# Optimization experiments

Hardware: AMD Instinct MI355X
Metric: run time of the kernel (lower is better)

Reference implementation:

```python
import jax, jax.numpy as jnp
import numpy as np

B, N_KERNELS, IN_DIM, UNITS = 512, 128, 1024, 1024

def setup_inputs() -> dict:
    key = jax.random.key(0)
    k1, k2 = jax.random.split(key)
    x = jax.random.normal(k1, (B, N_KERNELS, IN_DIM), dtype=jnp.float32)
    kernels = jax.random.normal(k2, (N_KERNELS, IN_DIM, UNITS), dtype=jnp.float32) * 0.02
    return {"x": x, "kernels": kernels}

def reference(x, kernels):
    # Original loops over n_kernels doing x[:, i:i+1, :] @ kernels[i] then softplus.
    # Note: the original's K.bias_add return value is discarded, so bias never
    # affects the output; the faithful math has no bias term.
    # Batched GEMM over the position axis k: [B,K,I] x [K,I,O] -> [B,K,O]
    out = jax.nn.softplus(jnp.einsum('bki,kio->bko', x, kernels))
    return out
```

## Files before the change

### kernel.cpp

```cpp
#include <hip/hip_runtime.h>

#define NKER  128
#define INDIM 1024
#define UNITS 1024

typedef __attribute__((ext_vector_type(8)))  short          bf16x8;
typedef __attribute__((ext_vector_type(4)))  float          f32x4;
typedef __attribute__((ext_vector_type(4)))  unsigned short u16x4;
typedef __attribute__((ext_vector_type(8)))  unsigned short u16x8;

#define LGKM0   asm volatile("s_waitcnt lgkmcnt(0)" ::: "memory")
#define BAR()   __builtin_amdgcn_s_barrier()
#define SCHED0  __builtin_amdgcn_sched_barrier(0)

__device__ __forceinline__ unsigned short f2bf(float f) {
    return __builtin_bit_cast(unsigned short, static_cast<__bf16>(f));
}

__device__ __forceinline__ int swzidx(int r, int k) {
    return r * 32 + ((((k >> 3) ^ ((r >> 1) & 3)) << 3) | (k & 7));
}

__global__ void __launch_bounds__(512, 2)
dense_local(const float* __restrict__ X, const float* __restrict__ Kn,
            float* __restrict__ Out)
{
    __shared__ __align__(16) unsigned short lA[2][2][256 * 32];
    __shared__ __align__(16) unsigned short lB[2][2][128 * 32];

    const int bid  = blockIdx.x;
    const int wg   = (bid & 7) * 256 + (bid >> 3);
    const int kidx = wg >> 4;
    const int tile = wg & 15;
    const int mt   = tile >> 3;
    const int nt   = tile & 7;

    const int t   = threadIdx.x;
    const int l   = t & 63;
    const int w   = t >> 6;
    const int wm  = w >> 1;
    const int wn  = w & 1;
    const int l15 = l & 15, g = l >> 4;

    const size_t MROW = (size_t)NKER * INDIM;

    const float* Abase = X   + (size_t)mt * 256 * MROW + (size_t)kidx * INDIM;
    const float* Bbase = Kn  + (size_t)kidx * INDIM * UNITS + nt * 128;
    float*       Cbase = Out + (size_t)mt * 256 * MROW + (size_t)kidx * UNITS + nt * 128;

    const int ar0 = t >> 3;
    const int ak4 = (t & 7) << 2;
    const int bn  = t & 127;
    const int bkh = t >> 7;

    const float* aP = Abase + (size_t)ar0 * MROW + ak4;
    const float* bP = Bbase + (size_t)bkh * 8 * UNITS + bn;

    f32x4 acc[4][4];
#pragma unroll
    for (int mi = 0; mi < 4; ++mi)
#pragma unroll
        for (int ni = 0; ni < 4; ++ni)
            acc[mi][ni] = f32x4{0.f, 0.f, 0.f, 0.f};

    f32x4 SA[4][2];
    float SB[2][8];

    auto issueA = [&]() {
#pragma unroll
        for (int p = 0; p < 4; ++p)
#pragma unroll
            for (int s = 0; s < 2; ++s)
                SA[p][s] = *(const f32x4*)(aP + (size_t)p * 64 * MROW + s * 32);
        aP += 64;
    };
    auto issueB = [&]() {
#pragma unroll
        for (int s = 0; s < 2; ++s)
#pragma unroll
            for (int j = 0; j < 8; ++j)
                SB[s][j] = bP[(size_t)(s * 32 + j) * UNITS];
        bP += (size_t)64 * UNITS;
    };
    auto cvtWriteA = [&](int nb) {
#pragma unroll
        for (int p = 0; p < 4; ++p)
#pragma unroll
            for (int s = 0; s < 2; ++s) {
                u16x4 h;
#pragma unroll
                for (int c = 0; c < 4; ++c) h[c] = f2bf(SA[p][s][c]);
                *(u16x4*)&lA[nb][s][swzidx(ar0 + p * 64, ak4)] = h;
            }
    };
    auto cvtWriteB = [&](int nb) {
#pragma unroll
        for (int s = 0; s < 2; ++s) {
            u16x8 h;
#pragma unroll
            for (int j = 0; j < 8; ++j) h[j] = f2bf(SB[s][j]);
            *(u16x8*)&lB[nb][s][swzidx(bn, bkh * 8)] = h;
        }
    };

    auto body = [&](int tt, bool wr, bool iss) {
        const int c = tt & 1, nb = c ^ 1;
        bf16x8 af0[4], bf0[4], af1[4], bf1[4];
#pragma unroll
        for (int mi = 0; mi < 4; ++mi)
            af0[mi] = *(const bf16x8*)&lA[c][0][swzidx(wm * 64 + mi * 16 + l15, g * 8)];
#pragma unroll
        for (int ni = 0; ni < 4; ++ni)
            bf0[ni] = *(const bf16x8*)&lB[c][0][swzidx(wn * 64 + ni * 16 + l15, g * 8)];
        if (wr)  cvtWriteA(nb);
        if (iss) issueA();
        BAR();
        LGKM0; SCHED0;
        __builtin_amdgcn_s_setprio(1);
#pragma unroll
        for (int mi = 0; mi < 4; ++mi)
#pragma unroll
            for (int ni = 0; ni < 4; ++ni)
                acc[mi][ni] = __builtin_amdgcn_mfma_f32_16x16x32_bf16(
                    af0[mi], bf0[ni], acc[mi][ni], 0, 0, 0);
        __builtin_amdgcn_s_setprio(0);
        BAR();
#pragma unroll
        for (int mi = 0; mi < 4; ++mi)
            af1[mi] = *(const bf16x8*)&lA[c][1][swzidx(wm * 64 + mi * 16 + l15, g * 8)];
#pragma unroll
        for (int ni = 0; ni < 4; ++ni)
            bf1[ni] = *(const bf16x8*)&lB[c][1][swzidx(wn * 64 + ni * 16 + l15, g * 8)];
        if (wr)  cvtWriteB(nb);
        if (iss) issueB();
        BAR();
        LGKM0; SCHED0;
        __builtin_amdgcn_s_setprio(1);
#pragma unroll
        for (int mi = 0; mi < 4; ++mi)
#pragma unroll
            for (int ni = 0; ni < 4; ++ni)
                acc[mi][ni] = __builtin_amdgcn_mfma_f32_16x16x32_bf16(
                    af1[mi], bf1[ni], acc[mi][ni], 0, 0, 0);
        __builtin_amdgcn_s_setprio(0);
        BAR();
    };

    issueA();
    issueB();
    cvtWriteA(0);
    issueA();
    cvtWriteB(0);
    issueB();
    LGKM0;
    BAR();

#pragma unroll 1
    for (int tt = 0; tt < 14; ++tt)
        body(tt, true, true);
    body(14, true, false);
    body(15, false, false);

#pragma unroll
    for (int mi = 0; mi < 4; ++mi) {
#pragma unroll
        for (int ni = 0; ni < 4; ++ni) {
            const int n = wn * 64 + ni * 16 + l15;
#pragma unroll
            for (int r = 0; r < 4; ++r) {
                const int m = wm * 64 + mi * 16 + g * 4 + r;
                const float v  = acc[mi][ni][r];
                const float sp = fmaxf(v, 0.0f) + log1pf(__expf(-fabsf(v)));
                Cbase[(size_t)m * MROW + n] = sp;
            }
        }
    }
}

extern "C" void kernel_launch(void* const* d_in, const int* in_sizes, int n_in,
                              void* d_out, int out_size, void* d_ws, size_t ws_size,
                              hipStream_t stream) {
    const float* X  = (const float*)d_in[0];
    const float* Kn = (const float*)d_in[1];
    float* O = (float*)d_out;
    dense_local<<<2048, 512, 0, stream>>>(X, Kn, O);
}
```

Measured before the change: 474.0 us.

## Merge two half-k phases into one phase with a single barrier per tile

Loads both k-halves of A and B fragments from LDS up front, performs the convert-and-write of the next buffer and the global prefetch together, then runs all 32 MFMAs in one block. The iteration now has one barrier instead of four, and the waitcnt loses its memory clobber. This removes synchronization stalls at the cost of more live fragment registers and less interleaving of LDS traffic with MFMA work.

```diff
diff --git a/kernel.cpp b/kernel.cpp
--- a/kernel.cpp
+++ b/kernel.cpp
@@ -9,7 +9,7 @@
 typedef __attribute__((ext_vector_type(4)))  unsigned short u16x4;
 typedef __attribute__((ext_vector_type(8)))  unsigned short u16x8;
 
-#define LGKM0   asm volatile("s_waitcnt lgkmcnt(0)" ::: "memory")
+#define LGKM0   asm volatile("s_waitcnt lgkmcnt(0)")
 #define BAR()   __builtin_amdgcn_s_barrier()
 #define SCHED0  __builtin_amdgcn_sched_barrier(0)
 
@@ -105,54 +105,41 @@
 
     auto body = [&](int tt, bool wr, bool iss) {
         const int c = tt & 1, nb = c ^ 1;
-        bf16x8 af0[4], bf0[4], af1[4], bf1[4];
-#pragma unroll
-        for (int mi = 0; mi < 4; ++mi)
-            af0[mi] = *(const bf16x8*)&lA[c][0][swzidx(wm * 64 + mi * 16 + l15, g * 8)];
-#pragma unroll
-        for (int ni = 0; ni < 4; ++ni)
-            bf0[ni] = *(const bf16x8*)&lB[c][0][swzidx(wn * 64 + ni * 16 + l15, g * 8)];
-        if (wr)  cvtWriteA(nb);
-        if (iss) issueA();
-        BAR();
-        LGKM0; SCHED0;
-        __builtin_amdgcn_s_setprio(1);
+        bf16x8 af[4][2], bfv[4][2];
 #pragma unroll
         for (int mi = 0; mi < 4; ++mi)
 #pragma unroll
-            for (int ni = 0; ni < 4; ++ni)
-                acc[mi][ni] = __builtin_amdgcn_mfma_f32_16x16x32_bf16(
-                    af0[mi], bf0[ni], acc[mi][ni], 0, 0, 0);
-        __builtin_amdgcn_s_setprio(0);
-        BAR();
-#pragma unroll
-        for (int mi = 0; mi < 4; ++mi)
-            af1[mi] = *(const bf16x8*)&lA[c][1][swzidx(wm * 64 + mi * 16 + l15, g * 8)];
+            for (int s = 0; s < 2; ++s)
+                af[mi][s] = *(const bf16x8*)&lA[c][s][swzidx(wm * 64 + mi * 16 + l15, g * 8)];
 #pragma unroll
         for (int ni = 0; ni < 4; ++ni)
-            bf1[ni] = *(const bf16x8*)&lB[c][1][swzidx(wn * 64 + ni * 16 + l15, g * 8)];
-        if (wr)  cvtWriteB(nb);
-        if (iss) issueB();
-        BAR();
-        LGKM0; SCHED0;
+#pragma unroll
+            for (int s = 0; s < 2; ++s)
+                bfv[ni][s] = *(const bf16x8*)&lB[c][s][swzidx(wn * 64 + ni * 16 + l15, g * 8)];
+        if (wr)  { cvtWriteA(nb); cvtWriteB(nb); }
+        if (iss) { issueA(); issueB(); }
         __builtin_amdgcn_s_setprio(1);
 #pragma unroll
-        for (int mi = 0; mi < 4; ++mi)
+        for (int s = 0; s < 2; ++s)
 #pragma unroll
-            for (int ni = 0; ni < 4; ++ni)
-                acc[mi][ni] = __builtin_amdgcn_mfma_f32_16x16x32_bf16(
-                    af1[mi], bf1[ni], acc[mi][ni], 0, 0, 0);
+            for (int mi = 0; mi < 4; ++mi)
+#pragma unroll
+                for (int ni = 0; ni < 4; ++ni)
+                    acc[mi][ni] = __builtin_amdgcn_mfma_f32_16x16x32_bf16(
+                        af[mi][s], bfv[ni][s], acc[mi][ni], 0, 0, 0);
         __builtin_amdgcn_s_setprio(0);
+        SCHED0;
+        LGKM0;
+        SCHED0;
         BAR();
     };
 
-    issueA();
-    issueB();
-    cvtWriteA(0);
-    issueA();
-    cvtWriteB(0);
-    issueB();
+    issueA(); issueB();
+    cvtWriteA(0); cvtWriteB(0);
+    issueA(); issueB();
+    SCHED0;
     LGKM0;
+    SCHED0;
     BAR();
 
 #pragma unroll 1
```

After: 480.7 us. No clear change (+1.4%).
